# Performance work log

Measured on AMD Instinct MI355X. Metric: run time of the kernel, lower is better.

Reference implementation:

```python
import jax, jax.numpy as jnp
import numpy as np

B, N, D, H = 4, 1024, 512, 8
DH = D // H  # per-head dim for V and for each of the two Q/K halves
LAM = 0.5


def setup_inputs() -> dict:
    key = jax.random.key(0)
    ks = jax.random.split(key, 7)
    s = 0.02
    return {
        "x": jax.random.normal(ks[0], (B, N, D), dtype=jnp.float32),
        "Wq": jax.random.normal(ks[1], (D, 2 * D), dtype=jnp.float32) * s,
        "bq": jax.random.normal(ks[2], (2 * D,), dtype=jnp.float32) * s,
        "Wk": jax.random.normal(ks[3], (D, 2 * D), dtype=jnp.float32) * s,
        "bk": jax.random.normal(ks[4], (2 * D,), dtype=jnp.float32) * s,
        "Wv": jax.random.normal(ks[5], (D, D), dtype=jnp.float32) * s,
        "bv": jax.random.normal(ks[6], (D,), dtype=jnp.float32) * s,
    }


def reference(x, Wq, bq, Wk, bk, Wv, bv):
    b, n, d = x.shape
    q = (x @ Wq + bq).reshape(b, n, H, 2 * DH).transpose(0, 2, 1, 3)  # [B,H,N,2*DH]
    k = (x @ Wk + bk).reshape(b, n, H, 2 * DH).transpose(0, 2, 1, 3)
    v = (x @ Wv + bv).reshape(b, n, H, DH).transpose(0, 2, 1, 3)      # [B,H,N,DH]
    q1, q2 = q[..., :DH], q[..., DH:]
    k1, k2 = k[..., :DH], k[..., DH:]
    scale = 1.0 / jnp.sqrt(jnp.float32(DH))
    a1 = jax.nn.softmax(jnp.einsum("bhqd,bhkd->bhqk", q1, k1) * scale, axis=-1)
    a2 = jax.nn.softmax(jnp.einsum("bhqd,bhkd->bhqk", q2, k2) * scale, axis=-1)
    attn = a1 - LAM * a2                                              # [B,H,N,N]
    out = jnp.einsum("bhqk,bhkd->bhqd", attn, v)                      # [B,H,N,DH]
    return out.transpose(0, 2, 1, 3).reshape(b, n, d)
```

## Files before the change

kernel.cpp:

```cpp
#include <hip/hip_runtime.h>
#include <hip/hip_bf16.h>

typedef unsigned short u16;
typedef unsigned int u32;
typedef short s16x8 __attribute__((ext_vector_type(8)));
typedef short s16x4 __attribute__((ext_vector_type(4)));
typedef float f32x4 __attribute__((ext_vector_type(4)));

__device__ inline u16 f2bf(float f) {
  union { float f; unsigned int u; } v; v.f = f;
  unsigned int r = v.u + 0x7fffu + ((v.u >> 16) & 1u);
  return (u16)(r >> 16);
}

__device__ __forceinline__ u32 cvt_pk_bf16(float lo, float hi) {
  u32 r;
  asm("v_cvt_pk_bf16_f32 %0, %1, %2" : "=v"(r) : "v"(lo), "v"(hi));
  return r;
}

__device__ __forceinline__ void g2lds16(const u16* g, u16* l) {
  __builtin_amdgcn_global_load_lds((const __attribute__((address_space(1))) void*)g,
                                   (__attribute__((address_space(3))) void*)l, 16, 0, 0);
}

__global__ __launch_bounds__(256) void cast_x_kernel(const float* __restrict__ x,
                                                     u16* __restrict__ xb) {
  int i = (blockIdx.x * 256 + threadIdx.x) * 8;
  float4 a = *(const float4*)(x + i);
  float4 b = *(const float4*)(x + i + 4);
  s16x8 o;
  o[0] = (short)f2bf(a.x); o[1] = (short)f2bf(a.y);
  o[2] = (short)f2bf(a.z); o[3] = (short)f2bf(a.w);
  o[4] = (short)f2bf(b.x); o[5] = (short)f2bf(b.y);
  o[6] = (short)f2bf(b.z); o[7] = (short)f2bf(b.w);
  *(s16x8*)(xb + i) = o;
}

__global__ __launch_bounds__(256) void transpose_cast_w_all(const float* __restrict__ Wq,
                                                            const float* __restrict__ Wk,
                                                            const float* __restrict__ Wv,
                                                            u16* __restrict__ wt) {
  __shared__ float tile[64][65];
  int jg = blockIdx.x * 64;
  const float* src; int C, j0;
  if (jg < 1024)      { src = Wq; C = 1024; j0 = jg; }
  else if (jg < 2048) { src = Wk; C = 1024; j0 = jg - 1024; }
  else                { src = Wv; C = 512;  j0 = jg - 2048; }
  int k0 = blockIdx.y * 64;
  int tx = threadIdx.x % 64, ty4 = threadIdx.x / 64;
#pragma unroll
  for (int p = 0; p < 16; ++p) {
    int r = p * 4 + ty4;
    tile[r][tx] = src[(size_t)(k0 + r) * C + j0 + tx];
  }
  __syncthreads();
#pragma unroll
  for (int p = 0; p < 16; ++p) {
    int r = p * 4 + ty4;
    wt[(size_t)(jg + r) * 512 + k0 + tx] = f2bf(tile[tx][r]);
  }
}

__global__ __launch_bounds__(256, 2) void gemm_qkv(const u16* __restrict__ xb, const u16* __restrict__ wt,
                                                   const float* __restrict__ bq, const float* __restrict__ bk,
                                                   const float* __restrict__ bv,
                                                   u16* __restrict__ qa, u16* __restrict__ ka,
                                                   u16* __restrict__ va) {
  __shared__ __align__(16) u16 As[128 * 64];
  __shared__ __align__(16) u16 Bs[128 * 64];
  int m0 = blockIdx.x * 128, j0 = blockIdx.y * 128;
  int tid = threadIdx.x;
  int w = tid >> 6, lane = tid & 63, quad = lane >> 4, l16 = lane & 15;
  int wr = (w >> 1) * 64, wc = (w & 1) * 64;

  int srow[4], scol[4], sbase[4];
#pragma unroll
  for (int it = 0; it < 4; ++it) {
    int s = it * 256 + tid;
    srow[it] = s >> 3;
    scol[it] = (s & 7) ^ ((s >> 3) & 7);
    sbase[it] = (s & ~63) * 8;
  }

  f32x4 acc[4][4];
#pragma unroll
  for (int i = 0; i < 4; ++i)
#pragma unroll
    for (int j = 0; j < 4; ++j)
#pragma unroll
      for (int r = 0; r < 4; ++r) acc[i][j][r] = 0.f;

  for (int kk = 0; kk < 8; ++kk) {
    int k0 = kk * 64;
    __syncthreads();
#pragma unroll
    for (int it = 0; it < 4; ++it) {
      g2lds16(xb + (size_t)(m0 + srow[it]) * 512 + k0 + scol[it] * 8, &As[sbase[it]]);
      g2lds16(wt + (size_t)(j0 + srow[it]) * 512 + k0 + scol[it] * 8, &Bs[sbase[it]]);
    }
    __syncthreads();
#pragma unroll
    for (int kb = 0; kb < 2; ++kb) {
      s16x8 af[4], bfr[4];
#pragma unroll
      for (int rb = 0; rb < 4; ++rb) {
        int row = wr + rb * 16 + l16;
        af[rb] = *(const s16x8*)(&As[row * 64 + (((kb * 4 + quad) ^ (row & 7)) * 8)]);
      }
#pragma unroll
      for (int cb = 0; cb < 4; ++cb) {
        int row = wc + cb * 16 + l16;
        bfr[cb] = *(const s16x8*)(&Bs[row * 64 + (((kb * 4 + quad) ^ (row & 7)) * 8)]);
      }
#pragma unroll
      for (int rb = 0; rb < 4; ++rb)
#pragma unroll
        for (int cb = 0; cb < 4; ++cb)
          acc[rb][cb] = __builtin_amdgcn_mfma_f32_16x16x32_bf16(af[rb], bfr[cb], acc[rb][cb], 0, 0, 0);
    }
  }

#pragma unroll
  for (int cb = 0; cb < 4; ++cb) {
    int j = j0 + wc + cb * 16 + l16;
    float bias = (j < 1024) ? bq[j] : (j < 2048) ? bk[j - 1024] : bv[j - 2048];
#pragma unroll
    for (int rb = 0; rb < 4; ++rb) {
#pragma unroll
      for (int r = 0; r < 4; ++r) {
        int m = m0 + wr + rb * 16 + quad * 4 + r;
        int bidx = m >> 10, n = m & 1023;
        u16 o = f2bf(acc[rb][cb][r] + bias);
        if (j < 1024) {
          int h = j >> 7, r2 = j & 127;
          qa[((size_t)((bidx * 8 + h) * 1024 + n)) * 128 + r2] = o;
        } else if (j < 2048) {
          int jj = j - 1024, h = jj >> 7, r2 = jj & 127;
          ka[((size_t)((bidx * 8 + h) * 1024 + n)) * 128 + r2] = o;
        } else {
          int jj = j - 2048, h = jj >> 6, d = jj & 63;
          va[((size_t)((bidx * 8 + h) * 64 + d)) * 1024 + n] = o;
        }
      }
    }
  }
}

__global__ __launch_bounds__(256, 2) void attn_kernel(const u16* __restrict__ qa, const u16* __restrict__ ka,
                                                      const u16* __restrict__ va, float* __restrict__ out) {
  __shared__ __align__(16) u16 Ks[2][64 * 128];
  __shared__ __align__(16) u16 Vs[2][64 * 64];
  int bh = blockIdx.x, b = bh >> 3, h = bh & 7;
  int q0 = blockIdx.y * 64;
  int tid = threadIdx.x, w = tid >> 6, lane = tid & 63, quad = lane >> 4, l16 = lane & 15;

  const u16* qrow = qa + (size_t)(bh * 1024 + q0 + w * 16 + l16) * 128;
  s16x8 qf[2][2];
  qf[0][0] = *(const s16x8*)(qrow + quad * 8);
  qf[0][1] = *(const s16x8*)(qrow + 32 + quad * 8);
  qf[1][0] = *(const s16x8*)(qrow + 64 + quad * 8);
  qf[1][1] = *(const s16x8*)(qrow + 96 + quad * 8);

  f32x4 O1[5], O2[5];
#pragma unroll
  for (int i = 0; i < 5; ++i)
#pragma unroll
    for (int r = 0; r < 4; ++r) { O1[i][r] = 0.f; O2[i][r] = 0.f; }

  s16x8 onesf;
#pragma unroll
  for (int i = 0; i < 8; ++i) onesf[i] = (l16 == 0) ? (short)0x3F80 : (short)0;

  int krow[4], kcol[4], kbse[4];
#pragma unroll
  for (int it = 0; it < 4; ++it) {
    int s = it * 256 + tid;
    krow[it] = s >> 4; kcol[it] = (s & 15) ^ ((s >> 4) & 7); kbse[it] = (s & ~63) * 8;
  }
  int vrow[2], vcol[2], vbse[2];
#pragma unroll
  for (int it = 0; it < 2; ++it) {
    int s = it * 256 + tid;
    vrow[it] = s >> 3; vcol[it] = (s & 7) ^ ((s >> 3) & 7); vbse[it] = (s & ~63) * 8;
  }
  const u16* kgbase = ka + (size_t)bh * 1024 * 128;
  const u16* vgbase = va + (size_t)bh * 64 * 1024;

  auto stageK = [&](int n0, u16* Kd) {
#pragma unroll
    for (int it = 0; it < 4; ++it)
      g2lds16(kgbase + (size_t)(n0 + krow[it]) * 128 + kcol[it] * 8, Kd + kbse[it]);
  };
  auto stageV = [&](int n0, u16* Vd) {
#pragma unroll
    for (int it = 0; it < 2; ++it)
      g2lds16(vgbase + (size_t)vrow[it] * 1024 + n0 + vcol[it] * 8, Vd + vbse[it]);
  };

  stageK(0, &Ks[0][0]);
  stageV(0, &Vs[0][0]);
  __syncthreads();

  for (int kt = 0; kt < 16; ++kt) {
    int cur = kt & 1;
    if (kt < 15) { stageK((kt + 1) * 64, &Ks[cur ^ 1][0]); stageV((kt + 1) * 64, &Vs[cur ^ 1][0]); }

    const u16* KsC = &Ks[cur][0];
    f32x4 sv[2][4];
#pragma unroll
    for (int hh = 0; hh < 2; ++hh)
#pragma unroll
      for (int nt = 0; nt < 4; ++nt) {
        f32x4 a; a[0] = a[1] = a[2] = a[3] = 0.f;
#pragma unroll
        for (int kb = 0; kb < 2; ++kb) {
          int row = nt * 16 + l16;
          s16x8 kf = *(const s16x8*)(&KsC[row * 128 + (((hh * 8 + kb * 4 + quad) ^ (row & 7)) * 8)]);
          a = __builtin_amdgcn_mfma_f32_16x16x32_bf16(kf, qf[hh][kb], a, 0, 0, 0);
        }
        sv[hh][nt] = a;
      }

    const u16* VsC = &Vs[cur][0];
    s16x8 vB[4][2];
#pragma unroll
    for (int ct = 0; ct < 4; ++ct) {
      int row = ct * 16 + l16, rx = row & 7;
#pragma unroll
      for (int hf = 0; hf < 2; ++hf) {
        union { s16x4 hl[2]; s16x8 v; } u;
#pragma unroll
        for (int j = 0; j < 2; ++j) {
          int nt = 2 * hf + j;
          int lc = 2 * nt + (quad >> 1);
          u.hl[j] = *(const s16x4*)(&VsC[row * 64 + (((lc ^ rx) << 3) + ((quad & 1) << 2))]);
        }
        vB[ct][hf] = u.v;
      }
    }

    s16x8 pA[2][2];
#pragma unroll
    for (int hh = 0; hh < 2; ++hh)
#pragma unroll
      for (int hf = 0; hf < 2; ++hf) {
        union { u32 wd[4]; s16x8 v; } u;
#pragma unroll
        for (int j = 0; j < 2; ++j) {
          int nt = 2 * hf + j;
          float e0 = __builtin_exp2f(sv[hh][nt][0] * 0.18033688f);
          float e1 = __builtin_exp2f(sv[hh][nt][1] * 0.18033688f);
          float e2 = __builtin_exp2f(sv[hh][nt][2] * 0.18033688f);
          float e3 = __builtin_exp2f(sv[hh][nt][3] * 0.18033688f);
          u.wd[2 * j]     = cvt_pk_bf16(e0, e1);
          u.wd[2 * j + 1] = cvt_pk_bf16(e2, e3);
        }
        pA[hh][hf] = u.v;
      }

#pragma unroll
    for (int ct = 0; ct < 5; ++ct)
#pragma unroll
      for (int hf = 0; hf < 2; ++hf) {
        s16x8 bf = (ct < 4) ? vB[ct][hf] : onesf;
        O1[ct] = __builtin_amdgcn_mfma_f32_16x16x32_bf16(pA[0][hf], bf, O1[ct], 0, 0, 0);
        O2[ct] = __builtin_amdgcn_mfma_f32_16x16x32_bf16(pA[1][hf], bf, O2[ct], 0, 0, 0);
      }

    __syncthreads();
  }

  float inv1[4], inv2[4];
#pragma unroll
  for (int r = 0; r < 4; ++r) {
    float l1 = __shfl(O1[4][r], lane & 48, 64);
    float l2 = __shfl(O2[4][r], lane & 48, 64);
    inv1[r] = 1.0f / l1;
    inv2[r] = 1.0f / l2;
  }
  int nb = q0 + w * 16 + quad * 4;
#pragma unroll
  for (int ct = 0; ct < 4; ++ct)
#pragma unroll
    for (int r = 0; r < 4; ++r) {
      float val = O1[ct][r] * inv1[r] - 0.5f * O2[ct][r] * inv2[r];
      out[(size_t)(b * 1024 + nb + r) * 512 + h * 64 + ct * 16 + l16] = val;
    }
}

extern "C" void kernel_launch(void* const* d_in, const int* in_sizes, int n_in,
                              void* d_out, int out_size, void* d_ws, size_t ws_size,
                              hipStream_t stream) {
  (void)in_sizes; (void)n_in; (void)out_size; (void)ws_size;
  const float* x  = (const float*)d_in[0];
  const float* Wq = (const float*)d_in[1];
  const float* bq = (const float*)d_in[2];
  const float* Wk = (const float*)d_in[3];
  const float* bk = (const float*)d_in[4];
  const float* Wv = (const float*)d_in[5];
  const float* bv = (const float*)d_in[6];
  float* out = (float*)d_out;

  char* ws = (char*)d_ws;
  u16* xb = (u16*)(ws);
  u16* wt = (u16*)(ws + 4194304);
  u16* qa = (u16*)(ws + 6815744);
  u16* ka = (u16*)(ws + 15204352);
  u16* va = (u16*)(ws + 23592960);

  cast_x_kernel<<<1024, 256, 0, stream>>>(x, xb);
  transpose_cast_w_all<<<dim3(40, 8), 256, 0, stream>>>(Wq, Wk, Wv, wt);
  gemm_qkv<<<dim3(32, 20), 256, 0, stream>>>(xb, wt, bq, bk, bv, qa, ka, va);
  attn_kernel<<<dim3(32, 16), 256, 0, stream>>>(qa, ka, va, out);
}
```

Before: 134.9 us.

## Split attention key range across two wave groups with LDS reduction

```diff
diff --git a/kernel.cpp b/kernel.cpp
--- a/kernel.cpp
+++ b/kernel.cpp
@@ -147,15 +147,19 @@
   }
 }
 
-__global__ __launch_bounds__(256, 2) void attn_kernel(const u16* __restrict__ qa, const u16* __restrict__ ka,
+__global__ __launch_bounds__(512, 4) void attn_kernel(const u16* __restrict__ qa, const u16* __restrict__ ka,
                                                       const u16* __restrict__ va, float* __restrict__ out) {
-  __shared__ __align__(16) u16 Ks[2][64 * 128];
-  __shared__ __align__(16) u16 Vs[2][64 * 64];
+  __shared__ __align__(16) u16 smem[40960];
   int bh = blockIdx.x, b = bh >> 3, h = bh & 7;
   int q0 = blockIdx.y * 64;
   int tid = threadIdx.x, w = tid >> 6, lane = tid & 63, quad = lane >> 4, l16 = lane & 15;
-
-  const u16* qrow = qa + (size_t)(bh * 1024 + q0 + w * 16 + l16) * 128;
+  int hfid = w >> 2, lw = w & 3, t256 = tid & 255;
+  u16* hb = smem + hfid * 20480;
+  u16* const KbA = hb;
+  u16* const KbB = hb + 8192;
+  u16* const Vsb = hb + 16384;
+
+  const u16* qrow = qa + (size_t)(bh * 1024 + q0 + lw * 16 + l16) * 128;
   s16x8 qf[2][2];
   qf[0][0] = *(const s16x8*)(qrow + quad * 8);
   qf[0][1] = *(const s16x8*)(qrow + 32 + quad * 8);
@@ -175,38 +179,39 @@
   int krow[4], kcol[4], kbse[4];
 #pragma unroll
   for (int it = 0; it < 4; ++it) {
-    int s = it * 256 + tid;
+    int s = it * 256 + t256;
     krow[it] = s >> 4; kcol[it] = (s & 15) ^ ((s >> 4) & 7); kbse[it] = (s & ~63) * 8;
   }
   int vrow[2], vcol[2], vbse[2];
 #pragma unroll
   for (int it = 0; it < 2; ++it) {
-    int s = it * 256 + tid;
+    int s = it * 256 + t256;
     vrow[it] = s >> 3; vcol[it] = (s & 7) ^ ((s >> 3) & 7); vbse[it] = (s & ~63) * 8;
   }
   const u16* kgbase = ka + (size_t)bh * 1024 * 128;
   const u16* vgbase = va + (size_t)bh * 64 * 1024;
+  int nbase = hfid * 512;
 
   auto stageK = [&](int n0, u16* Kd) {
 #pragma unroll
     for (int it = 0; it < 4; ++it)
       g2lds16(kgbase + (size_t)(n0 + krow[it]) * 128 + kcol[it] * 8, Kd + kbse[it]);
   };
-  auto stageV = [&](int n0, u16* Vd) {
+  auto stageV = [&](int n0) {
 #pragma unroll
     for (int it = 0; it < 2; ++it)
-      g2lds16(vgbase + (size_t)vrow[it] * 1024 + n0 + vcol[it] * 8, Vd + vbse[it]);
+      g2lds16(vgbase + (size_t)vrow[it] * 1024 + n0 + vcol[it] * 8, Vsb + vbse[it]);
   };
 
-  stageK(0, &Ks[0][0]);
-  stageV(0, &Vs[0][0]);
+  stageK(nbase, KbA);
+  stageV(nbase);
   __syncthreads();
 
-  for (int kt = 0; kt < 16; ++kt) {
-    int cur = kt & 1;
-    if (kt < 15) { stageK((kt + 1) * 64, &Ks[cur ^ 1][0]); stageV((kt + 1) * 64, &Vs[cur ^ 1][0]); }
-
-    const u16* KsC = &Ks[cur][0];
+  for (int kt = 0; kt < 8; ++kt) {
+    u16* const KsC = (kt & 1) ? KbB : KbA;
+    u16* const KsN = (kt & 1) ? KbA : KbB;
+    if (kt < 7) stageK(nbase + (kt + 1) * 64, KsN);
+
     f32x4 sv[2][4];
 #pragma unroll
     for (int hh = 0; hh < 2; ++hh)
@@ -222,7 +227,6 @@
         sv[hh][nt] = a;
       }
 
-    const u16* VsC = &Vs[cur][0];
     s16x8 vB[4][2];
 #pragma unroll
     for (int ct = 0; ct < 4; ++ct) {
@@ -234,11 +238,14 @@
         for (int j = 0; j < 2; ++j) {
           int nt = 2 * hf + j;
           int lc = 2 * nt + (quad >> 1);
-          u.hl[j] = *(const s16x4*)(&VsC[row * 64 + (((lc ^ rx) << 3) + ((quad & 1) << 2))]);
+          u.hl[j] = *(const s16x4*)(&Vsb[row * 64 + (((lc ^ rx) << 3) + ((quad & 1) << 2))]);
         }
         vB[ct][hf] = u.v;
       }
     }
+
+    asm volatile("s_waitcnt lgkmcnt(0)\n\ts_barrier" ::: "memory");
+    if (kt < 7) stageV(nbase + (kt + 1) * 64);
 
     s16x8 pA[2][2];
 #pragma unroll
@@ -271,22 +278,40 @@
     __syncthreads();
   }
 
-  float inv1[4], inv2[4];
-#pragma unroll
-  for (int r = 0; r < 4; ++r) {
-    float l1 = __shfl(O1[4][r], lane & 48, 64);
-    float l2 = __shfl(O2[4][r], lane & 48, 64);
-    inv1[r] = 1.0f / l1;
-    inv2[r] = 1.0f / l2;
-  }
-  int nb = q0 + w * 16 + quad * 4;
-#pragma unroll
-  for (int ct = 0; ct < 4; ++ct)
+  float* scr = (float*)smem;
+  if (w >= 4) {
+    int base = (w - 4) * 2560 + lane * 4;
+#pragma unroll
+    for (int i = 0; i < 5; ++i) {
+      *(f32x4*)&scr[base + i * 256]       = O1[i];
+      *(f32x4*)&scr[base + (i + 5) * 256] = O2[i];
+    }
+  }
+  __syncthreads();
+  if (w < 4) {
+    int base = w * 2560 + lane * 4;
+#pragma unroll
+    for (int i = 0; i < 5; ++i) {
+      O1[i] += *(const f32x4*)&scr[base + i * 256];
+      O2[i] += *(const f32x4*)&scr[base + (i + 5) * 256];
+    }
+    float inv1[4], inv2[4];
 #pragma unroll
     for (int r = 0; r < 4; ++r) {
-      float val = O1[ct][r] * inv1[r] - 0.5f * O2[ct][r] * inv2[r];
-      out[(size_t)(b * 1024 + nb + r) * 512 + h * 64 + ct * 16 + l16] = val;
-    }
+      float l1 = __shfl(O1[4][r], lane & 48, 64);
+      float l2 = __shfl(O2[4][r], lane & 48, 64);
+      inv1[r] = 1.0f / l1;
+      inv2[r] = 1.0f / l2;
+    }
+    int nb = q0 + w * 16 + quad * 4;
+#pragma unroll
+    for (int ct = 0; ct < 4; ++ct)
+#pragma unroll
+      for (int r = 0; r < 4; ++r) {
+        float val = O1[ct][r] * inv1[r] - 0.5f * O2[ct][r] * inv2[r];
+        out[(size_t)(b * 1024 + nb + r) * 512 + h * 64 + ct * 16 + l16] = val;
+      }
+  }
 }
 
 extern "C" void kernel_launch(void* const* d_in, const int* in_sizes, int n_in,
@@ -312,5 +337,5 @@
   cast_x_kernel<<<1024, 256, 0, stream>>>(x, xb);
   transpose_cast_w_all<<<dim3(40, 8), 256, 0, stream>>>(Wq, Wk, Wv, wt);
   gemm_qkv<<<dim3(32, 20), 256, 0, stream>>>(xb, wt, bq, bk, bv, qa, ka, va);
-  attn_kernel<<<dim3(32, 16), 256, 0, stream>>>(qa, ka, va, out);
-}
+  attn_kernel<<<dim3(32, 16), 512, 0, stream>>>(qa, ka, va, out);
+}
```

Result: slower. 147.9 us (+9.6%).
